# Optimization experiments

Measured on AMD Instinct MI355X. Metric: run time of the kernel, lower is better.

The kernel has to match this reference:

```python
import jax, jax.numpy as jnp
import numpy as np

B, T, C, H = 4, 2048, 1024, 16
HD = C // H  # head dim = 64


def _rope(x, pos):
    """Rotary embedding. x: [B,H,T,hd], pos: [B,T] int positions."""
    half = x.shape[-1] // 2
    inv_freq = 1.0 / (10000.0 ** (jnp.arange(half, dtype=jnp.float32) / half))
    ang = pos.astype(jnp.float32)[:, None, :, None] * inv_freq  # [B,1,T,half]
    cos, sin = jnp.cos(ang), jnp.sin(ang)
    x1, x2 = x[..., :half], x[..., half:]
    return jnp.concatenate([x1 * cos - x2 * sin, x1 * sin + x2 * cos], axis=-1)


def setup_inputs() -> dict:
    key = jax.random.key(0)
    k1, k2, k3 = jax.random.split(key, 3)
    x = jax.random.normal(k1, (B, T, C), dtype=jnp.float32)
    W_attn = jax.random.normal(k2, (C, 3 * C), dtype=jnp.float32) * (1.0 / np.sqrt(C))
    W_proj = jax.random.normal(k3, (C, C), dtype=jnp.float32) * (1.0 / np.sqrt(C))
    indices = jnp.broadcast_to(jnp.arange(T, dtype=jnp.int32)[None, :], (B, T))
    return {"x": x, "W_attn": W_attn, "W_proj": W_proj, "indices": indices}


def reference(x, W_attn, W_proj, indices):
    # QKV projection (bias=False)
    qkv = x @ W_attn  # [B,T,3C]
    q, k, v = jnp.split(qkv, 3, axis=-1)

    def to_heads(t):
        return t.reshape(B, T, H, HD).transpose(0, 2, 1, 3)  # [B,H,T,hd]

    q, k, v = to_heads(q), to_heads(k), to_heads(v)
    # RoPE on q and k at positions given by indices (pos_emb_closure.adapt_*)
    q = _rope(q, indices)
    k = _rope(k, indices)

    # attn_mask = k_indices <= q_indices, shape [B,1,T,T]
    mask = indices[:, None, None, :] <= indices[:, None, :, None]

    att = jnp.einsum("bhqd,bhkd->bhqk", q, k) * (1.0 / np.sqrt(HD))
    att = jnp.where(mask, att, jnp.float32(-jnp.inf))
    att = jax.nn.softmax(att, axis=-1)
    y = jnp.einsum("bhqk,bhkd->bhqd", att, v)  # [B,H,T,hd]
    y = y.transpose(0, 2, 1, 3).reshape(B, T, C)
    return y @ W_proj
```

## Files before the change

kernel.cpp:

```cpp
#include <hip/hip_runtime.h>
#include <math.h>

namespace {
constexpr int Bsz = 4;
constexpr int T   = 2048;
constexpr int C   = 1024;
constexpr int H   = 16;
constexpr int HD  = 64;

typedef short bf16x8 __attribute__((ext_vector_type(8)));
typedef float f32x4  __attribute__((ext_vector_type(4)));

#if defined(__has_builtin)
#if __has_builtin(__builtin_amdgcn_global_load_lds)
#define HAVE_GLL 1
typedef __attribute__((address_space(3))) unsigned int lds_u32_t;
typedef __attribute__((address_space(1))) unsigned int g_u32_t;
#define GLL16(gp, lp)                                                        \
  __builtin_amdgcn_global_load_lds((const g_u32_t*)(gp), (lds_u32_t*)(lp),   \
                                   16, 0, 0)
#endif
#endif

__device__ __forceinline__ unsigned short f2bf(float f) {
  unsigned int u = __builtin_bit_cast(unsigned int, f);
  u += 0x7FFFu + ((u >> 16) & 1u);
  return (unsigned short)(u >> 16);
}
__device__ __forceinline__ float bf2f(unsigned short s) {
  unsigned int u = ((unsigned int)s) << 16;
  return __builtin_bit_cast(float, u);
}
__device__ __forceinline__ unsigned int cvtpk_bf16(float a, float b) {
  unsigned int r;
  asm("v_cvt_pk_bf16_f32 %0, %1, %2" : "=v"(r) : "v"(a), "v"(b));
  return r;
}

__global__ __launch_bounds__(256) void f32_to_bf16_kernel(
    const float* __restrict__ in, unsigned short* __restrict__ out, int n4) {
  int i = blockIdx.x * 256 + threadIdx.x;
  if (i < n4) {
    float4 v = ((const float4*)in)[i];
    ushort4 o;
    o.x = f2bf(v.x); o.y = f2bf(v.y); o.z = f2bf(v.z); o.w = f2bf(v.w);
    ((ushort4*)out)[i] = o;
  }
}

__global__ __launch_bounds__(256) void transpose_bf16_kernel(
    const float* __restrict__ W, unsigned short* __restrict__ Wt, int K, int N) {
  __shared__ float tile[32][33];
  const int n0 = blockIdx.x * 32, k0 = blockIdx.y * 32;
  const int r = threadIdx.x >> 3, c4 = threadIdx.x & 7;
  float4 v = *(const float4*)(W + (size_t)(k0 + r) * N + n0 + c4 * 4);
  tile[r][c4 * 4 + 0] = v.x;
  tile[r][c4 * 4 + 1] = v.y;
  tile[r][c4 * 4 + 2] = v.z;
  tile[r][c4 * 4 + 3] = v.w;
  __syncthreads();
  ushort4 o;
  o.x = f2bf(tile[c4 * 4 + 0][r]);
  o.y = f2bf(tile[c4 * 4 + 1][r]);
  o.z = f2bf(tile[c4 * 4 + 2][r]);
  o.w = f2bf(tile[c4 * 4 + 3][r]);
  *(ushort4*)(Wt + (size_t)(n0 + r) * K + k0 + c4 * 4) = o;
}

template <int MODE>
__global__ __launch_bounds__(256) void gemm_bt(
    const unsigned short* __restrict__ A, const unsigned short* __restrict__ Bt,
    float* __restrict__ Cout, unsigned short* __restrict__ qp,
    unsigned short* __restrict__ kp, unsigned short* __restrict__ vp,
    int M, int N, int K) {
  __shared__ __align__(16) unsigned short As[128 * 32];
  __shared__ __align__(16) unsigned short Bs[128 * 32];
  const int tid = threadIdx.x;
  const int lane = tid & 63, w = tid >> 6;
  const int wr = w & 1, wc = w >> 1;
  const int l15 = lane & 15, quad = lane >> 4;
  const int m0 = blockIdx.y * 128, n0 = blockIdx.x * 128;

  const int srow = lane >> 2;
  const int schunk = (lane & 3) * 8;
  const unsigned short* gA = A + (size_t)(m0 + w * 32 + srow) * K + schunk;
  const unsigned short* gB = Bt + (size_t)(n0 + w * 32 + srow) * K + schunk;
  unsigned short* lA0 = &As[(w * 32) * 32 + lane * 8];
  unsigned short* lA1 = &As[(w * 32 + 16) * 32 + lane * 8];
  unsigned short* lB0 = &Bs[(w * 32) * 32 + lane * 8];
  unsigned short* lB1 = &Bs[(w * 32 + 16) * 32 + lane * 8];

  f32x4 acc[4][4] = {};

  for (int k0 = 0; k0 < K; k0 += 32) {
    __syncthreads();
#ifdef HAVE_GLL
    GLL16(gA + k0, lA0);
    GLL16(gA + (size_t)16 * K + k0, lA1);
    GLL16(gB + k0, lB0);
    GLL16(gB + (size_t)16 * K + k0, lB1);
#else
    *(uint4*)lA0 = *(const uint4*)(gA + k0);
    *(uint4*)lA1 = *(const uint4*)(gA + (size_t)16 * K + k0);
    *(uint4*)lB0 = *(const uint4*)(gB + k0);
    *(uint4*)lB1 = *(const uint4*)(gB + (size_t)16 * K + k0);
#endif
    __syncthreads();

    bf16x8 af[4], bfr[4];
#pragma unroll
    for (int mf = 0; mf < 4; ++mf)
      af[mf] = *(const bf16x8*)&As[(wr * 64 + mf * 16 + l15) * 32 + quad * 8];
#pragma unroll
    for (int nf = 0; nf < 4; ++nf)
      bfr[nf] = *(const bf16x8*)&Bs[(wc * 64 + nf * 16 + l15) * 32 + quad * 8];
#pragma unroll
    for (int mf = 0; mf < 4; ++mf)
#pragma unroll
      for (int nf = 0; nf < 4; ++nf)
        acc[mf][nf] = __builtin_amdgcn_mfma_f32_16x16x32_bf16(
            af[mf], bfr[nf], acc[mf][nf], 0, 0, 0);
  }

#pragma unroll
  for (int mf = 0; mf < 4; ++mf) {
    const int row0 = m0 + wr * 64 + mf * 16 + quad * 4;
#pragma unroll
    for (int nf = 0; nf < 4; ++nf) {
      if (MODE == 0) {
#pragma unroll
        for (int r = 0; r < 4; ++r) {
          const int col = n0 + wc * 64 + nf * 16 + l15;
          Cout[(size_t)(row0 + r) * N + col] = acc[mf][nf][r];
        }
      } else {
        const int col = n0 + wc * 64 + nf * 16 + l15;
        const int which = col >> 10;
        const int rem = col & (C - 1);
        const int h = rem >> 6, hd = rem & 63;
        const int b = row0 >> 11, t0 = row0 & (T - 1);
        if (which == 2) {
          ushort4 pv;
          pv.x = f2bf(acc[mf][nf][0]);
          pv.y = f2bf(acc[mf][nf][1]);
          pv.z = f2bf(acc[mf][nf][2]);
          pv.w = f2bf(acc[mf][nf][3]);
          *(ushort4*)(vp + (((size_t)(b * H + h)) * HD + hd) * T + t0) = pv;
        } else {
          unsigned short* dst = which == 0 ? qp : kp;
#pragma unroll
          for (int r = 0; r < 4; ++r)
            dst[(((size_t)(b * H + h)) * T + t0 + r) * HD + hd] =
                f2bf(acc[mf][nf][r]);
        }
      }
    }
  }
}

__global__ __launch_bounds__(256) void rope_bf16(unsigned short* __restrict__ q,
                                                 unsigned short* __restrict__ k,
                                                 const int* __restrict__ idx) {
  const size_t g = (size_t)blockIdx.x * 8 + (threadIdx.x >> 5);
  const int lane = threadIdx.x & 31;
  const int t = (int)(g & (size_t)(T - 1));
  const int bh = (int)(g >> 11);
  const int b = bh >> 4;
  const int pos = idx[b * T + t];
  const float inv = 1.0f / powf(10000.0f, (float)lane * (1.0f / 32.0f));
  float sn, cs;
  sincosf((float)pos * inv, &sn, &cs);
  const float SC = 0.18033688f;
  const float snq = sn * SC, csq = cs * SC;
  const size_t base = g * (size_t)HD;
  float x1 = bf2f(q[base + lane]), x2 = bf2f(q[base + 32 + lane]);
  q[base + lane]      = f2bf(x1 * csq - x2 * snq);
  q[base + 32 + lane] = f2bf(x1 * snq + x2 * csq);
  x1 = bf2f(k[base + lane]);
  x2 = bf2f(k[base + 32 + lane]);
  k[base + lane]      = f2bf(x1 * cs - x2 * sn);
  k[base + 32 + lane] = f2bf(x1 * sn + x2 * cs);
}

__global__ __launch_bounds__(256) void flash_attn_mfma(
    const unsigned short* __restrict__ q, const unsigned short* __restrict__ k,
    const unsigned short* __restrict__ vt, const int* __restrict__ idx,
    unsigned short* __restrict__ y) {
  __shared__ __align__(16) unsigned short Ks[2][64][72];
  __shared__ __align__(16) unsigned short Vts[2][64][72];
  __shared__ __align__(16) unsigned short Pq[64][72];
  __shared__ int kmaxs[32];

  const int tid = threadIdx.x;
  const int lane = tid & 63, w = tid >> 6;
  const int l15 = lane & 15, quad = lane >> 4;

  const int flat = (blockIdx.z * H + blockIdx.y) * 16 + blockIdx.x;
  const int slot = flat >> 3;
  const int bh_i = (flat & 7) * 8 + (slot >> 4);
  const int bx = slot & 15;
  const int h = bh_i & (H - 1), b = bh_i >> 4;

  const size_t bh = (size_t)bh_i;
  const unsigned short* qg = q + bh * T * HD;
  const unsigned short* kg = k + bh * T * HD;
  const unsigned short* vg = vt + bh * HD * T;
  const int* idxb = idx + b * T;

  if (tid < 32) {
    const int4* p4 = (const int4*)(idxb + (tid << 6));
    int m = p4[0].x;
#pragma unroll
    for (int j = 0; j < 16; ++j) {
      int4 v = p4[j];
      m = max(m, max(max(v.x, v.y), max(v.z, v.w)));
    }
    kmaxs[tid] = m;
  }

  const int r1 = tid >> 3, c1 = tid & 7;
  const int r2 = r1 + 32;

  for (int ti = 0; ti < 2; ++ti) {
    const int qt = (ti == 0) ? bx : 31 - bx;
    const int q0 = qt * 64;
    const int qrow = q0 + w * 16 + l15;

    const bf16x8 bq0 = *(const bf16x8*)(qg + (size_t)qrow * HD + quad * 8);
    const bf16x8 bq1 = *(const bf16x8*)(qg + (size_t)qrow * HD + 32 + quad * 8);
    const int pq = idxb[qrow];
    int mq = pq;
    mq = min(mq, __shfl_xor(mq, 1));
    mq = min(mq, __shfl_xor(mq, 2));
    mq = min(mq, __shfl_xor(mq, 4));
    mq = min(mq, __shfl_xor(mq, 8));

    float m_run = -1e38f, l_run = 0.0f;
    f32x4 Oa[4] = {};

    {
      uint4 ka = *(const uint4*)(kg + (size_t)r1 * HD + c1 * 8);
      uint4 kb = *(const uint4*)(kg + (size_t)r2 * HD + c1 * 8);
      uint4 va = *(const uint4*)(vg + (size_t)r1 * T + c1 * 8);
      uint4 vb = *(const uint4*)(vg + (size_t)r2 * T + c1 * 8);
      __syncthreads();
      *(uint4*)&Ks[0][r1][c1 * 8] = ka;
      *(uint4*)&Ks[0][r2][c1 * 8] = kb;
      *(uint4*)&Vts[0][r1][c1 * 8] = va;
      *(uint4*)&Vts[0][r2][c1 * 8] = vb;
    }

    for (int kt = 0; kt <= qt; ++kt) {
      const int cur = kt & 1;
      const int k0 = kt * 64;
      __syncthreads();

      uint4 nka, nkb, nva, nvb;
      if (kt < qt) {
        const int kn = k0 + 64;
        nka = *(const uint4*)(kg + (size_t)(kn + r1) * HD + c1 * 8);
        nkb = *(const uint4*)(kg + (size_t)(kn + r2) * HD + c1 * 8);
        nva = *(const uint4*)(vg + (size_t)r1 * T + kn + c1 * 8);
        nvb = *(const uint4*)(vg + (size_t)r2 * T + kn + c1 * 8);
      }

      f32x4 Sa[4];
#pragma unroll
      for (int nf = 0; nf < 4; ++nf) {
        bf16x8 ak0 = *(const bf16x8*)&Ks[cur][nf * 16 + l15][quad * 8];
        bf16x8 ak1 = *(const bf16x8*)&Ks[cur][nf * 16 + l15][32 + quad * 8];
        f32x4 s = {};
        s = __builtin_amdgcn_mfma_f32_16x16x32_bf16(ak0, bq0, s, 0, 0, 0);
        s = __builtin_amdgcn_mfma_f32_16x16x32_bf16(ak1, bq1, s, 0, 0, 0);
        Sa[nf] = s;
      }

      if (kmaxs[kt] > mq) {
#pragma unroll
        for (int nf = 0; nf < 4; ++nf) {
          const int4 pk4 = *(const int4*)(idxb + k0 + nf * 16 + quad * 4);
          if (pk4.x > pq) Sa[nf][0] = -3e38f;
          if (pk4.y > pq) Sa[nf][1] = -3e38f;
          if (pk4.z > pq) Sa[nf][2] = -3e38f;
          if (pk4.w > pq) Sa[nf][3] = -3e38f;
        }
      }

      float m0 = fmaxf(fmaxf(Sa[0][0], Sa[0][1]), fmaxf(Sa[0][2], Sa[0][3]));
      float m1 = fmaxf(fmaxf(Sa[1][0], Sa[1][1]), fmaxf(Sa[1][2], Sa[1][3]));
      float m2 = fmaxf(fmaxf(Sa[2][0], Sa[2][1]), fmaxf(Sa[2][2], Sa[2][3]));
      float m3 = fmaxf(fmaxf(Sa[3][0], Sa[3][1]), fmaxf(Sa[3][2], Sa[3][3]));
      float mx = fmaxf(fmaxf(m0, m1), fmaxf(m2, m3));
      mx = fmaxf(mx, __shfl_xor(mx, 16));
      mx = fmaxf(mx, __shfl_xor(mx, 32));

      if (!__all(mx <= m_run + 8.0f)) {
        const float mn = fmaxf(m_run, mx);
        const float alpha = exp2f(m_run - mn);
        m_run = mn;
        l_run *= alpha;
#pragma unroll
        for (int nfd = 0; nfd < 4; ++nfd)
#pragma unroll
          for (int r = 0; r < 4; ++r) Oa[nfd][r] *= alpha;
      }

      float s0 = 0.f, s1 = 0.f, s2 = 0.f, s3 = 0.f;
#pragma unroll
      for (int nf = 0; nf < 4; ++nf) {
        float p0 = exp2f(Sa[nf][0] - m_run);
        float p1 = exp2f(Sa[nf][1] - m_run);
        float p2 = exp2f(Sa[nf][2] - m_run);
        float p3 = exp2f(Sa[nf][3] - m_run);
        Sa[nf][0] = p0; Sa[nf][1] = p1; Sa[nf][2] = p2; Sa[nf][3] = p3;
        s0 += p0; s1 += p1; s2 += p2; s3 += p3;
      }
      float sum = (s0 + s1) + (s2 + s3);
      sum += __shfl_xor(sum, 16);
      sum += __shfl_xor(sum, 32);
      l_run += sum;

#pragma unroll
      for (int nf = 0; nf < 4; ++nf) {
        uint2 pw;
        pw.x = cvtpk_bf16(Sa[nf][0], Sa[nf][1]);
        pw.y = cvtpk_bf16(Sa[nf][2], Sa[nf][3]);
        *(uint2*)&Pq[w * 16 + l15][nf * 16 + quad * 4] = pw;
      }

      asm volatile("s_waitcnt lgkmcnt(0)" ::: "memory");

      const bf16x8 bp0 = *(const bf16x8*)&Pq[w * 16 + l15][quad * 8];
      const bf16x8 bp1 = *(const bf16x8*)&Pq[w * 16 + l15][32 + quad * 8];

#pragma unroll
      for (int nfd = 0; nfd < 4; ++nfd) {
        bf16x8 av0 = *(const bf16x8*)&Vts[cur][nfd * 16 + l15][quad * 8];
        bf16x8 av1 = *(const bf16x8*)&Vts[cur][nfd * 16 + l15][32 + quad * 8];
        Oa[nfd] = __builtin_amdgcn_mfma_f32_16x16x32_bf16(av0, bp0, Oa[nfd], 0, 0, 0);
        Oa[nfd] = __builtin_amdgcn_mfma_f32_16x16x32_bf16(av1, bp1, Oa[nfd], 0, 0, 0);
      }

      if (kt < qt) {
        const int nxt = cur ^ 1;
        *(uint4*)&Ks[nxt][r1][c1 * 8] = nka;
        *(uint4*)&Ks[nxt][r2][c1 * 8] = nkb;
        *(uint4*)&Vts[nxt][r1][c1 * 8] = nva;
        *(uint4*)&Vts[nxt][r2][c1 * 8] = nvb;
      }
    }

    const float rl = 1.0f / l_run;
    const size_t base = ((size_t)b * T + qrow) * (size_t)C + h * HD;
#pragma unroll
    for (int nfd = 0; nfd < 4; ++nfd) {
      ushort4 o;
      o.x = f2bf(Oa[nfd][0] * rl);
      o.y = f2bf(Oa[nfd][1] * rl);
      o.z = f2bf(Oa[nfd][2] * rl);
      o.w = f2bf(Oa[nfd][3] * rl);
      *(ushort4*)(y + base + nfd * 16 + quad * 4) = o;
    }
  }
}

}

extern "C" void kernel_launch(void* const* d_in, const int* in_sizes, int n_in,
                              void* d_out, int out_size, void* d_ws,
                              size_t ws_size, hipStream_t stream) {
  const float* x      = (const float*)d_in[0];
  const float* W_attn = (const float*)d_in[1];
  const float* W_proj = (const float*)d_in[2];
  const int* indices  = (const int*)d_in[3];
  float* out = (float*)d_out;

  const size_t nM = (size_t)Bsz * T * C;
  unsigned short* xb  = (unsigned short*)d_ws;
  unsigned short* wat = xb + nM;
  unsigned short* wpt = wat + (size_t)3 * C * C;
  unsigned short* qp  = wpt + (size_t)C * C;
  unsigned short* kp  = qp + nM;
  unsigned short* vp  = kp + nM;
  unsigned short* yb  = vp + nM;

  f32_to_bf16_kernel<<<(int)(nM / 4 / 256), 256, 0, stream>>>(x, xb, (int)(nM / 4));
  transpose_bf16_kernel<<<dim3(3 * C / 32, C / 32), 256, 0, stream>>>(W_attn, wat, C, 3 * C);
  transpose_bf16_kernel<<<dim3(C / 32, C / 32), 256, 0, stream>>>(W_proj, wpt, C, C);
  gemm_bt<1><<<dim3(3 * C / 128, Bsz * T / 128), 256, 0, stream>>>(
      xb, wat, nullptr, qp, kp, vp, Bsz * T, 3 * C, C);
  rope_bf16<<<(Bsz * H * T) / 8, 256, 0, stream>>>(qp, kp, indices);
  flash_attn_mfma<<<dim3(16, H, Bsz), 256, 0, stream>>>(qp, kp, vp, indices, yb);
  gemm_bt<0><<<dim3(C / 128, Bsz * T / 128), 256, 0, stream>>>(
      yb, wpt, out, nullptr, nullptr, nullptr, Bsz * T, C, C);
}
```

Measured before the change: 327.2 us.

## Swizzle attention LDS tiles, add MFMA priority, and reuse RoPE angles across heads

The attention kernel drops the padded 72-wide LDS rows for unpadded 64-wide rows with an XOR swizzle on the column index, which removes the padding and is meant to avoid bank conflicts. It brackets the MFMA loops with s_setprio and replaces the shared kmaxs array with per-lane max values fetched by wavefront shuffle. The RoPE kernel now computes sin/cos once per (batch, position) and loops over all 16 heads, with exp2f replacing powf for the inverse frequency. Risks are swizzle-correctness bugs and lower parallelism in RoPE, since the grid is 16x smaller.

```diff
diff --git a/kernel.cpp b/kernel.cpp
--- a/kernel.cpp
+++ b/kernel.cpp
@@ -161,35 +161,36 @@
 __global__ __launch_bounds__(256) void rope_bf16(unsigned short* __restrict__ q,
                                                  unsigned short* __restrict__ k,
                                                  const int* __restrict__ idx) {
-  const size_t g = (size_t)blockIdx.x * 8 + (threadIdx.x >> 5);
+  const int g = blockIdx.x * 8 + (threadIdx.x >> 5);
   const int lane = threadIdx.x & 31;
-  const int t = (int)(g & (size_t)(T - 1));
-  const int bh = (int)(g >> 11);
-  const int b = bh >> 4;
+  const int b = g >> 11, t = g & (T - 1);
   const int pos = idx[b * T + t];
-  const float inv = 1.0f / powf(10000.0f, (float)lane * (1.0f / 32.0f));
+  const float inv = exp2f((float)lane * -0.41524101186f);
   float sn, cs;
   sincosf((float)pos * inv, &sn, &cs);
   const float SC = 0.18033688f;
   const float snq = sn * SC, csq = cs * SC;
-  const size_t base = g * (size_t)HD;
-  float x1 = bf2f(q[base + lane]), x2 = bf2f(q[base + 32 + lane]);
-  q[base + lane]      = f2bf(x1 * csq - x2 * snq);
-  q[base + 32 + lane] = f2bf(x1 * snq + x2 * csq);
-  x1 = bf2f(k[base + lane]);
-  x2 = bf2f(k[base + 32 + lane]);
-  k[base + lane]      = f2bf(x1 * cs - x2 * sn);
-  k[base + 32 + lane] = f2bf(x1 * sn + x2 * cs);
+  const size_t base0 = ((size_t)b * H * T + t) * HD + lane;
+#pragma unroll 4
+  for (int h = 0; h < H; ++h) {
+    const size_t base = base0 + (size_t)h * T * HD;
+    float x1 = bf2f(q[base]), x2 = bf2f(q[base + 32]);
+    q[base]      = f2bf(x1 * csq - x2 * snq);
+    q[base + 32] = f2bf(x1 * snq + x2 * csq);
+    x1 = bf2f(k[base]);
+    x2 = bf2f(k[base + 32]);
+    k[base]      = f2bf(x1 * cs - x2 * sn);
+    k[base + 32] = f2bf(x1 * sn + x2 * cs);
+  }
 }
 
 __global__ __launch_bounds__(256) void flash_attn_mfma(
     const unsigned short* __restrict__ q, const unsigned short* __restrict__ k,
     const unsigned short* __restrict__ vt, const int* __restrict__ idx,
     unsigned short* __restrict__ y) {
-  __shared__ __align__(16) unsigned short Ks[2][64][72];
-  __shared__ __align__(16) unsigned short Vts[2][64][72];
-  __shared__ __align__(16) unsigned short Pq[64][72];
-  __shared__ int kmaxs[32];
+  __shared__ __align__(16) unsigned short Ks[2][64 * 64];
+  __shared__ __align__(16) unsigned short Vts[2][64 * 64];
+  __shared__ __align__(16) unsigned short Pq[64 * 64];
 
   const int tid = threadIdx.x;
   const int lane = tid & 63, w = tid >> 6;
@@ -207,19 +208,24 @@
   const unsigned short* vg = vt + bh * HD * T;
   const int* idxb = idx + b * T;
 
-  if (tid < 32) {
-    const int4* p4 = (const int4*)(idxb + (tid << 6));
-    int m = p4[0].x;
-#pragma unroll
-    for (int j = 0; j < 16; ++j) {
+  int km;
+  {
+    const int4* p4 = (const int4*)(idxb + (lane << 5));
+    int4 v0 = p4[0];
+    int m = max(max(v0.x, v0.y), max(v0.z, v0.w));
+#pragma unroll
+    for (int j = 1; j < 8; ++j) {
       int4 v = p4[j];
       m = max(m, max(max(v.x, v.y), max(v.z, v.w)));
     }
-    kmaxs[tid] = m;
+    km = max(m, __shfl_xor(m, 1));
   }
 
   const int r1 = tid >> 3, c1 = tid & 7;
   const int r2 = r1 + 32;
+  const int swS1 = r1 * 64 + ((c1 * 8) ^ ((r1 & 7) << 3));
+  const int swS2 = r2 * 64 + ((c1 * 8) ^ ((r1 & 7) << 3));
+  const int rx = (l15 & 7) << 3;
 
   for (int ti = 0; ti < 2; ++ti) {
     const int qt = (ti == 0) ? bx : 31 - bx;
@@ -244,10 +250,10 @@
       uint4 va = *(const uint4*)(vg + (size_t)r1 * T + c1 * 8);
       uint4 vb = *(const uint4*)(vg + (size_t)r2 * T + c1 * 8);
       __syncthreads();
-      *(uint4*)&Ks[0][r1][c1 * 8] = ka;
-      *(uint4*)&Ks[0][r2][c1 * 8] = kb;
-      *(uint4*)&Vts[0][r1][c1 * 8] = va;
-      *(uint4*)&Vts[0][r2][c1 * 8] = vb;
+      *(uint4*)&Ks[0][swS1] = ka;
+      *(uint4*)&Ks[0][swS2] = kb;
+      *(uint4*)&Vts[0][swS1] = va;
+      *(uint4*)&Vts[0][swS2] = vb;
     }
 
     for (int kt = 0; kt <= qt; ++kt) {
@@ -265,17 +271,21 @@
       }
 
       f32x4 Sa[4];
+      __builtin_amdgcn_s_setprio(1);
 #pragma unroll
       for (int nf = 0; nf < 4; ++nf) {
-        bf16x8 ak0 = *(const bf16x8*)&Ks[cur][nf * 16 + l15][quad * 8];
-        bf16x8 ak1 = *(const bf16x8*)&Ks[cur][nf * 16 + l15][32 + quad * 8];
+        const int row = (nf * 16 + l15) * 64;
+        bf16x8 ak0 = *(const bf16x8*)&Ks[cur][row + ((quad * 8) ^ rx)];
+        bf16x8 ak1 = *(const bf16x8*)&Ks[cur][row + ((32 + quad * 8) ^ rx)];
         f32x4 s = {};
         s = __builtin_amdgcn_mfma_f32_16x16x32_bf16(ak0, bq0, s, 0, 0, 0);
         s = __builtin_amdgcn_mfma_f32_16x16x32_bf16(ak1, bq1, s, 0, 0, 0);
         Sa[nf] = s;
       }
-
-      if (kmaxs[kt] > mq) {
+      __builtin_amdgcn_s_setprio(0);
+
+      const int kmt = __shfl(km, kt << 1);
+      if (kmt > mq) {
 #pragma unroll
         for (int nf = 0; nf < 4; ++nf) {
           const int4 pk4 = *(const int4*)(idxb + k0 + nf * 16 + quad * 4);
@@ -286,11 +296,12 @@
         }
       }
 
-      float m0 = fmaxf(fmaxf(Sa[0][0], Sa[0][1]), fmaxf(Sa[0][2], Sa[0][3]));
-      float m1 = fmaxf(fmaxf(Sa[1][0], Sa[1][1]), fmaxf(Sa[1][2], Sa[1][3]));
-      float m2 = fmaxf(fmaxf(Sa[2][0], Sa[2][1]), fmaxf(Sa[2][2], Sa[2][3]));
-      float m3 = fmaxf(fmaxf(Sa[3][0], Sa[3][1]), fmaxf(Sa[3][2], Sa[3][3]));
-      float mx = fmaxf(fmaxf(m0, m1), fmaxf(m2, m3));
+      float mx = fmaxf(
+          fmaxf(fmaxf(fmaxf(Sa[0][0], Sa[0][1]), Sa[0][2]),
+                fmaxf(fmaxf(Sa[0][3], Sa[1][0]), Sa[1][1])),
+          fmaxf(fmaxf(fmaxf(Sa[1][2], Sa[1][3]), Sa[2][0]),
+                fmaxf(fmaxf(Sa[2][1], Sa[2][2]), Sa[2][3])));
+      mx = fmaxf(mx, fmaxf(fmaxf(Sa[3][0], Sa[3][1]), fmaxf(Sa[3][2], Sa[3][3])));
       mx = fmaxf(mx, __shfl_xor(mx, 16));
       mx = fmaxf(mx, __shfl_xor(mx, 32));
 
@@ -320,33 +331,40 @@
       sum += __shfl_xor(sum, 32);
       l_run += sum;
 
-#pragma unroll
-      for (int nf = 0; nf < 4; ++nf) {
-        uint2 pw;
-        pw.x = cvtpk_bf16(Sa[nf][0], Sa[nf][1]);
-        pw.y = cvtpk_bf16(Sa[nf][2], Sa[nf][3]);
-        *(uint2*)&Pq[w * 16 + l15][nf * 16 + quad * 4] = pw;
+      {
+        const int prow = (w * 16 + l15) * 64;
+#pragma unroll
+        for (int nf = 0; nf < 4; ++nf) {
+          uint2 pw;
+          pw.x = cvtpk_bf16(Sa[nf][0], Sa[nf][1]);
+          pw.y = cvtpk_bf16(Sa[nf][2], Sa[nf][3]);
+          *(uint2*)&Pq[prow + ((nf * 16 + quad * 4) ^ rx)] = pw;
+        }
       }
 
       asm volatile("s_waitcnt lgkmcnt(0)" ::: "memory");
 
-      const bf16x8 bp0 = *(const bf16x8*)&Pq[w * 16 + l15][quad * 8];
-      const bf16x8 bp1 = *(const bf16x8*)&Pq[w * 16 + l15][32 + quad * 8];
-
+      const int prow = (w * 16 + l15) * 64;
+      const bf16x8 bp0 = *(const bf16x8*)&Pq[prow + ((quad * 8) ^ rx)];
+      const bf16x8 bp1 = *(const bf16x8*)&Pq[prow + ((32 + quad * 8) ^ rx)];
+
+      __builtin_amdgcn_s_setprio(1);
 #pragma unroll
       for (int nfd = 0; nfd < 4; ++nfd) {
-        bf16x8 av0 = *(const bf16x8*)&Vts[cur][nfd * 16 + l15][quad * 8];
-        bf16x8 av1 = *(const bf16x8*)&Vts[cur][nfd * 16 + l15][32 + quad * 8];
+        const int vrow = (nfd * 16 + l15) * 64;
+        bf16x8 av0 = *(const bf16x8*)&Vts[cur][vrow + ((quad * 8) ^ rx)];
+        bf16x8 av1 = *(const bf16x8*)&Vts[cur][vrow + ((32 + quad * 8) ^ rx)];
         Oa[nfd] = __builtin_amdgcn_mfma_f32_16x16x32_bf16(av0, bp0, Oa[nfd], 0, 0, 0);
         Oa[nfd] = __builtin_amdgcn_mfma_f32_16x16x32_bf16(av1, bp1, Oa[nfd], 0, 0, 0);
       }
+      __builtin_amdgcn_s_setprio(0);
 
       if (kt < qt) {
         const int nxt = cur ^ 1;
-        *(uint4*)&Ks[nxt][r1][c1 * 8] = nka;
-        *(uint4*)&Ks[nxt][r2][c1 * 8] = nkb;
-        *(uint4*)&Vts[nxt][r1][c1 * 8] = nva;
-        *(uint4*)&Vts[nxt][r2][c1 * 8] = nvb;
+        *(uint4*)&Ks[nxt][swS1] = nka;
+        *(uint4*)&Ks[nxt][swS2] = nkb;
+        *(uint4*)&Vts[nxt][swS1] = nva;
+        *(uint4*)&Vts[nxt][swS2] = nvb;
       }
     }
 
@@ -389,7 +407,7 @@
   transpose_bf16_kernel<<<dim3(C / 32, C / 32), 256, 0, stream>>>(W_proj, wpt, C, C);
   gemm_bt<1><<<dim3(3 * C / 128, Bsz * T / 128), 256, 0, stream>>>(
       xb, wat, nullptr, qp, kp, vp, Bsz * T, 3 * C, C);
-  rope_bf16<<<(Bsz * H * T) / 8, 256, 0, stream>>>(qp, kp, indices);
+  rope_bf16<<<(Bsz * T) / 8, 256, 0, stream>>>(qp, kp, indices);
   flash_attn_mfma<<<dim3(16, H, Bsz), 256, 0, stream>>>(qp, kp, vp, indices, yb);
   gemm_bt<0><<<dim3(C / 128, Bsz * T / 128), 256, 0, stream>>>(
       yb, wpt, out, nullptr, nullptr, nullptr, Bsz * T, C, C);
```

Result: faster. 313.0 us (-4.3%).
